# Performance work log

Measured on AMD Instinct MI355X. Metric: run time of the kernel, lower is better.

## Reference

```python
import jax, jax.numpy as jnp
import numpy as np

N = 2048
IMG = 128
FOCAL = float(IMG)


def quat_to_rot(q):
    # q = (w, x, y, z), normalized -> (N, 3, 3) rotation matrices
    q = q / jnp.linalg.norm(q, axis=-1, keepdims=True)
    w, x, y, z = q[..., 0], q[..., 1], q[..., 2], q[..., 3]
    R = jnp.stack([
        1 - 2 * (y * y + z * z), 2 * (x * y - w * z), 2 * (x * z + w * y),
        2 * (x * y + w * z), 1 - 2 * (x * x + z * z), 2 * (y * z - w * x),
        2 * (x * z - w * y), 2 * (y * z + w * x), 1 - 2 * (x * x + y * y),
    ], axis=-1).reshape(q.shape[:-1] + (3, 3))
    return R


def setup_inputs() -> dict:
    key = jax.random.key(0)
    ks = jax.random.split(key, 4)
    return {
        'means': jax.random.normal(ks[0], (N, 3), jnp.float32) * 0.5,
        'log_scales': jnp.full((N, 3), -2.0, jnp.float32) + 0.1 * jax.random.normal(ks[1], (N, 3), jnp.float32),
        'rotations': jax.random.normal(ks[2], (N, 4), jnp.float32) + jnp.array([2.0, 0.0, 0.0, 0.0], jnp.float32),
        'opacity_logit': jnp.zeros((N, 1), jnp.float32),
        'color_pre': jax.random.normal(ks[3], (N, 3), jnp.float32) * 0.5,
        'cam_pos': jnp.array([0.0, 0.0, 5.0], jnp.float32),
        'look_at': jnp.zeros((3,), jnp.float32),
    }


def reference(means, log_scales, rotations, opacity_logit, color_pre, cam_pos, look_at):
    # --- activations of learned params ---
    scales = jnp.exp(log_scales)                      # (N, 3)
    opac = jax.nn.sigmoid(opacity_logit)[:, 0]        # (N,)
    colors = jax.nn.sigmoid(color_pre)                # (N, 3)

    # --- 3D covariance: Sigma = R S S^T R^T ---
    R = quat_to_rot(rotations)                        # (N, 3, 3)
    M = R * scales[:, None, :]                        # R @ diag(s)
    cov3d = M @ jnp.swapaxes(M, -1, -2)               # (N, 3, 3)

    # --- camera basis (world -> camera) ---
    fwd = look_at - cam_pos
    fwd = fwd / jnp.linalg.norm(fwd)
    right = jnp.cross(fwd, jnp.array([0.0, 1.0, 0.0], jnp.float32))
    right = right / jnp.linalg.norm(right)
    up = jnp.cross(right, fwd)
    Wm = jnp.stack([right, up, -fwd], axis=0)         # (3, 3)

    # --- project means ---
    means_cam = (means - cam_pos[None]) @ Wm.T        # (N, 3)
    depths = -means_cam[:, 2]
    x_cam = means_cam[:, 0] / (-means_cam[:, 2] + 1e-8)
    y_cam = means_cam[:, 1] / (-means_cam[:, 2] + 1e-8)
    means_2d = jnp.stack([x_cam * FOCAL + IMG / 2, -y_cam * FOCAL + IMG / 2], axis=-1)

    # --- EWA 2D covariance ---
    cov_cam = jnp.einsum('ab,nbc,dc->nad', Wm, cov3d, Wm)      # W Sigma W^T
    z_sq = jnp.maximum(depths ** 2, 0.01)[:, None, None]
    cov_2d = cov_cam[:, :2, :2] * FOCAL ** 2 / z_sq + 0.3 * jnp.eye(2, dtype=jnp.float32)

    # --- depth sort (front to back) ---
    idx = jnp.argsort(depths)
    d_s = depths[idx]
    m2d = means_2d[idx]
    c2d = cov_2d[idx]
    col_s = colors[idx]
    op_s = opac[idx]

    # culling -> mask instead of dynamic filtering (jit-friendly, same math)
    valid = ((d_s > 0.1)
             & (m2d[:, 0] > -IMG) & (m2d[:, 0] < 2 * IMG)
             & (m2d[:, 1] > -IMG) & (m2d[:, 1] < 2 * IMG)).astype(jnp.float32)

    a = c2d[:, 0, 0]
    b = c2d[:, 0, 1]
    d = c2d[:, 1, 1]
    det = jnp.maximum(a * d - b * b, 1e-6)
    cov_inv = jnp.stack([d, -b, -b, a], axis=-1).reshape(-1, 2, 2) / det[:, None, None]

    yy, xx = jnp.meshgrid(jnp.arange(IMG, dtype=jnp.float32),
                          jnp.arange(IMG, dtype=jnp.float32), indexing='ij')
    pixels = jnp.stack([xx, yy], axis=-1)             # (H, W, 2)

    def body(carry, g):
        image, T = carry
        mu, inv, col, op, v = g
        diff = pixels - mu                            # (H, W, 2)
        mahal = jnp.einsum('hwi,ij,hwj->hw', diff, inv, diff)
        alpha = jnp.minimum(op * jnp.exp(-0.5 * mahal), 0.99) * v
        image = image + (T * alpha)[..., None] * (col[None, None] - image)
        T = T * (1.0 - alpha)
        return (image, T), None

    init = (jnp.ones((IMG, IMG, 3), jnp.float32), jnp.ones((IMG, IMG), jnp.float32))
    (image, _), _ = jax.lax.scan(body, init, (m2d, cov_inv, col_s, op_s, valid))
    return jnp.clip(image, 0.0, 1.0)
```

## Files before the change

### kernel.cpp

```cpp
#include <hip/hip_runtime.h>
#include <hip/hip_bf16.h>
#include <hip/hip_fp16.h>

#define N_G   2048
#define IMGF  128.0f
#define RECF  8


typedef __fp16 half2_v __attribute__((ext_vector_type(2)));
union H2U { half2_v h2; float f; unsigned int u; };

static __device__ __forceinline__ unsigned int f32_bf16(float f) {
    unsigned int u = __float_as_uint(f);
    return (u + 0x7FFFu + ((u >> 16) & 1u)) >> 16;
}

__global__ void gs_preprocess(const float* __restrict__ means,
                              const float* __restrict__ log_scales,
                              const float* __restrict__ rotations,
                              const float* __restrict__ opacity_logit,
                              const float* __restrict__ color_pre,
                              const float* __restrict__ cam_pos,
                              const float* __restrict__ look_at,
                              float* __restrict__ rec,
                              unsigned long long* __restrict__ keys)
{
    int i = blockIdx.x * blockDim.x + threadIdx.x;
    if (i >= N_G) return;

    float cx = cam_pos[0], cy = cam_pos[1], cz = cam_pos[2];
    float fx = look_at[0] - cx, fy = look_at[1] - cy, fz = look_at[2] - cz;
    float fn = 1.0f / sqrtf(fx*fx + fy*fy + fz*fz);
    fx *= fn; fy *= fn; fz *= fn;
    float rx = -fz, ry = 0.0f, rz = fx;
    float rn = 1.0f / sqrtf(rx*rx + ry*ry + rz*rz);
    rx *= rn; ry *= rn; rz *= rn;
    float ux = ry*fz - rz*fy, uy = rz*fx - rx*fz, uz = rx*fy - ry*fx;

    float mx = means[3*i+0] - cx, my = means[3*i+1] - cy, mz = means[3*i+2] - cz;
    float m0 =  rx*mx + ry*my + rz*mz;
    float m1 =  ux*mx + uy*my + uz*mz;
    float m2 = -(fx*mx + fy*my + fz*mz);
    float d  = -m2;
    float invz = 1.0f / (-m2 + 1e-8f);
    float m2dx =  (m0 * invz) * IMGF + IMGF * 0.5f;
    float m2dy = -(m1 * invz) * IMGF + IMGF * 0.5f;

    float s0 = expf(log_scales[3*i+0]);
    float s1 = expf(log_scales[3*i+1]);
    float s2 = expf(log_scales[3*i+2]);
    float qw = rotations[4*i+0], qx = rotations[4*i+1],
          qy = rotations[4*i+2], qz = rotations[4*i+3];
    float qn = 1.0f / sqrtf(qw*qw + qx*qx + qy*qy + qz*qz);
    qw *= qn; qx *= qn; qy *= qn; qz *= qn;
    float R00 = 1-2*(qy*qy+qz*qz), R01 = 2*(qx*qy-qw*qz), R02 = 2*(qx*qz+qw*qy);
    float R10 = 2*(qx*qy+qw*qz), R11 = 1-2*(qx*qx+qz*qz), R12 = 2*(qy*qz-qw*qx);
    float R20 = 2*(qx*qz-qw*qy), R21 = 2*(qy*qz+qw*qx), R22 = 1-2*(qx*qx+qy*qy);
    float t0 = s0*s0, t1 = s1*s1, t2 = s2*s2;
    float C00 = R00*R00*t0 + R01*R01*t1 + R02*R02*t2;
    float C01 = R00*R10*t0 + R01*R11*t1 + R02*R12*t2;
    float C02 = R00*R20*t0 + R01*R21*t1 + R02*R22*t2;
    float C11 = R10*R10*t0 + R11*R11*t1 + R12*R12*t2;
    float C12 = R10*R20*t0 + R11*R21*t1 + R12*R22*t2;
    float C22 = R20*R20*t0 + R21*R21*t1 + R22*R22*t2;

    float v0 = C00*rx + C01*ry + C02*rz;
    float v1 = C01*rx + C11*ry + C12*rz;
    float v2 = C02*rx + C12*ry + C22*rz;
    float ca = rx*v0 + ry*v1 + rz*v2;
    float cb = ux*v0 + uy*v1 + uz*v2;
    float w0 = C00*ux + C01*uy + C02*uz;
    float w1 = C01*ux + C11*uy + C12*uz;
    float w2 = C02*ux + C12*uy + C22*uz;
    float cd = ux*w0 + uy*w1 + uz*w2;

    float z2 = fmaxf(d*d, 0.01f);
    float sc = (IMGF * IMGF) / z2;
    float a  = ca*sc + 0.3f;
    float b  = cb*sc;
    float dd = cd*sc + 0.3f;
    float det  = fmaxf(a*dd - b*b, 1e-6f);
    float idet = 1.0f / det;

    bool valid = (d > 0.1f) && (m2dx > -IMGF) && (m2dx < 2.0f*IMGF)
                            && (m2dy > -IMGF) && (m2dy < 2.0f*IMGF);

    float op = 1.0f / (1.0f + expf(-opacity_logit[i]));
    const float L2E = 1.4426950408889634f;
    float A2 = -0.5f * L2E * dd * idet;
    float B2 =          L2E * b  * idet;
    float D2 = -0.5f * L2E * a  * idet;
    float L  = valid ? log2f(op) : -1e10f;

    float cr = 1.0f / (1.0f + expf(-color_pre[3*i+0]));
    float cg = 1.0f / (1.0f + expf(-color_pre[3*i+1]));
    float cl = 1.0f / (1.0f + expf(-color_pre[3*i+2]));

    unsigned int w6 = f32_bf16(cr) | (f32_bf16(cg) << 16);
    unsigned int w7 = f32_bf16(cl);

    float4* r4 = (float4*)(rec + RECF*i);
    r4[0] = make_float4(m2dx, m2dy, A2, B2);
    r4[1] = make_float4(D2, L, __uint_as_float(w6), __uint_as_float(w7));

    unsigned int ub   = __float_as_uint(d);
    unsigned int mask = ((unsigned int)((int)ub >> 31)) | 0x80000000u;
    keys[i] = ((unsigned long long)(ub ^ mask) << 32) | (unsigned int)i;
}

__global__ void __launch_bounds__(256)
gs_rank_scatter(const unsigned long long* __restrict__ keys,
                const float* __restrict__ rec,
                float* __restrict__ srec)
{
    __shared__ __align__(16) unsigned long long sk[N_G];
    int t = threadIdx.x;

    const ulonglong2* k2 = (const ulonglong2*)keys;
    ulonglong2* s2 = (ulonglong2*)sk;
    #pragma unroll
    for (int q = 0; q < 4; ++q) s2[t + q*256] = k2[t + q*256];
    __syncthreads();

    int g   = (blockIdx.x << 5) | (t >> 3);
    int seg = t & 7;
    unsigned long long ki = sk[g];
    const ulonglong2* sseg = (const ulonglong2*)(sk + (seg << 8));
    int rank = 0;
    #pragma unroll 8
    for (int j = 0; j < 128; ++j) {
        ulonglong2 a = sseg[(j + seg * 17) & 127];
        rank += (int)(a.x < ki) + (int)(a.y < ki);
    }
    rank += __shfl_xor(rank, 1);
    rank += __shfl_xor(rank, 2);
    rank += __shfl_xor(rank, 4);

    int slot = ((rank & 31) << 6) | (rank >> 5);
    srec[slot * RECF + seg] = rec[g * RECF + seg];
}

__global__ void __launch_bounds__(256, 2)
gs_raster(const float* __restrict__ srec, float* __restrict__ out)
{
    int tid  = threadIdx.x;
    int lane = tid & 63;
    int wave = (blockIdx.x << 2) | (tid >> 6);
    int p0   = wave * 2;
    float px0 = (float)(p0 & 127);
    float px1 = px0 + 1.0f;
    float py  = (float)(p0 >> 7);

    float vp[32];
    float P0 = 1.0f, P1 = 1.0f;

    #pragma unroll
    for (int i = 0; i < 32; ++i) {
        const float* r = srec + (size_t)((i << 6) | lane) * RECF;
        float4 ra = *(const float4*)r;
        float2 rb = *(const float2*)(r + 4);
        float dy   = py - ra.y;
        float b2dy = ra.w * dy;
        float t2   = fmaf(rb.x * dy, dy, rb.y);
        float dx0  = px0 - ra.x;
        float dx1  = px1 - ra.x;
        float q0 = fmaf(dx0, fmaf(ra.z, dx0, b2dy), t2);
        float q1 = fmaf(dx1, fmaf(ra.z, dx1, b2dy), t2);
        float a0 = fminf(__builtin_amdgcn_exp2f(q0), 0.99f);
        float a1 = fminf(__builtin_amdgcn_exp2f(q1), 0.99f);
        float u0 = P0 * a0;  P0 *= (1.0f - a0);
        float u1 = P1 * a1;  P1 *= (1.0f - a1);
        H2U hp; hp.h2 = __builtin_amdgcn_cvt_pkrtz(u0, u1);
        vp[i] = hp.f;
    }

    float sp0 = P0, sp1 = P1;
    #pragma unroll
    for (int d = 1; d < 64; d <<= 1) {
        float y0 = __shfl_up(sp0, d);
        float y1 = __shfl_up(sp1, d);
        if (lane >= d) { sp0 *= y0; sp1 *= y1; }
    }
    float e0 = __shfl_up(sp0, 1);
    float e1 = __shfl_up(sp1, 1);
    float Tin0 = (lane == 0) ? 1.0f : e0;
    float Tin1 = (lane == 0) ? 1.0f : e1;

    float B0 = 1.0f, B1 = 1.0f;
    #pragma unroll
    for (int i = 0; i < 32; ++i) {
        H2U h; h.f = vp[i];
        B0 *= fmaf(-Tin0, (float)h.h2.x, 1.0f);
        B1 *= fmaf(-Tin1, (float)h.h2.y, 1.0f);
    }

    float ss0 = B0, ss1 = B1;
    #pragma unroll
    for (int d = 1; d < 64; d <<= 1) {
        float y0 = __shfl_down(ss0, d);
        float y1 = __shfl_down(ss1, d);
        if (lane + d < 64) { ss0 *= y0; ss1 *= y1; }
    }
    float f0 = __shfl_down(ss0, 1);
    float f1 = __shfl_down(ss1, 1);
    float S0 = (lane == 63) ? 1.0f : f0;
    float S1 = (lane == 63) ? 1.0f : f1;

    float ar0 = 0.0f, ag0 = 0.0f, ab0 = 0.0f;
    float ar1 = 0.0f, ag1 = 0.0f, ab1 = 0.0f;
    #pragma unroll
    for (int i = 31; i >= 0; --i) {
        const float* r = srec + (size_t)((i << 6) | lane) * RECF;
        float2 cp = *(const float2*)(r + 6);
        unsigned int w6 = __float_as_uint(cp.x);
        unsigned int w7 = __float_as_uint(cp.y);
        float cr = __uint_as_float(w6 << 16);
        float cg = __uint_as_float(w6 & 0xFFFF0000u);
        float cb = __uint_as_float(w7 << 16);
        H2U h; h.f = vp[i];
        float u0  = Tin0 * (float)h.h2.x;
        float us0 = u0 * S0;
        ar0 = fmaf(us0, cr, ar0); ag0 = fmaf(us0, cg, ag0); ab0 = fmaf(us0, cb, ab0);
        S0 = fmaf(-u0, S0, S0);
        float u1  = Tin1 * (float)h.h2.y;
        float us1 = u1 * S1;
        ar1 = fmaf(us1, cr, ar1); ag1 = fmaf(us1, cg, ag1); ab1 = fmaf(us1, cb, ab1);
        S1 = fmaf(-u1, S1, S1);
    }

    #pragma unroll
    for (int d = 1; d < 64; d <<= 1) {
        ar0 += __shfl_xor(ar0, d); ag0 += __shfl_xor(ag0, d); ab0 += __shfl_xor(ab0, d);
        ar1 += __shfl_xor(ar1, d); ag1 += __shfl_xor(ab1*0.0f + ag1, d); ab1 += __shfl_xor(ab1, d);
    }

    if (lane == 0) {
        float* o0 = out + (size_t)p0 * 3;
        o0[0] = fminf(fmaxf(S0 + ar0, 0.0f), 1.0f);
        o0[1] = fminf(fmaxf(S0 + ag0, 0.0f), 1.0f);
        o0[2] = fminf(fmaxf(S0 + ab0, 0.0f), 1.0f);
        o0[3] = fminf(fmaxf(S1 + ar1, 0.0f), 1.0f);
        o0[4] = fminf(fmaxf(S1 + ag1, 0.0f), 1.0f);
        o0[5] = fminf(fmaxf(S1 + ab1, 0.0f), 1.0f);
    }
}

extern "C" void kernel_launch(void* const* d_in, const int* in_sizes, int n_in,
                              void* d_out, int out_size, void* d_ws, size_t ws_size,
                              hipStream_t stream)
{
    const float* means         = (const float*)d_in[0];
    const float* log_scales    = (const float*)d_in[1];
    const float* rotations     = (const float*)d_in[2];
    const float* opacity_logit = (const float*)d_in[3];
    const float* color_pre     = (const float*)d_in[4];
    const float* cam_pos       = (const float*)d_in[5];
    const float* look_at       = (const float*)d_in[6];
    float* out = (float*)d_out;

    char* ws = (char*)d_ws;
    float*              rec  = (float*)(ws);
    unsigned long long* keys = (unsigned long long*)(ws + 65536);
    float*              srec = (float*)(ws + 65536 + 16384);

    hipLaunchKernelGGL(gs_preprocess, dim3(N_G / 256), dim3(256), 0, stream,
                       means, log_scales, rotations, opacity_logit, color_pre,
                       cam_pos, look_at, rec, keys);
    hipLaunchKernelGGL(gs_rank_scatter, dim3(N_G / 32), dim3(256), 0, stream,
                       keys, rec, srec);
    hipLaunchKernelGGL(gs_raster, dim3(2048), dim3(256), 0, stream,
                       srec, out);
}
```

Baseline: 106.3 us.

## Process gaussians in four sequential chunks of 512 with per-chunk wave scans

The raster kernel now splits the 2048 sorted gaussians into four chunks of 512, each with its own forward transmittance scan and backward suffix scan across the wave. Results are combined across chunks through carried transmittance and a suffix-product multiplier. The sort's slot mapping changes to match the chunked layout, and the separate B-product pass is dropped. This shrinks the per-thread vp register array from 32 to 8, which lowers register pressure and the occupancy hint is relaxed accordingly, but it adds four times as many cross-lane scan rounds.

```diff
diff --git a/kernel.cpp b/kernel.cpp
--- a/kernel.cpp
+++ b/kernel.cpp
@@ -136,11 +136,11 @@
     rank += __shfl_xor(rank, 2);
     rank += __shfl_xor(rank, 4);
 
-    int slot = ((rank & 31) << 6) | (rank >> 5);
+    int slot = (rank & ~511) | ((rank & 7) << 6) | ((rank >> 3) & 63);
     srec[slot * RECF + seg] = rec[g * RECF + seg];
 }
 
-__global__ void __launch_bounds__(256, 2)
+__global__ void __launch_bounds__(256)
 gs_raster(const float* __restrict__ srec, float* __restrict__ out)
 {
     int tid  = threadIdx.x;
@@ -151,97 +151,112 @@
     float px1 = px0 + 1.0f;
     float py  = (float)(p0 >> 7);
 
-    float vp[32];
-    float P0 = 1.0f, P1 = 1.0f;
-
-    #pragma unroll
-    for (int i = 0; i < 32; ++i) {
-        const float* r = srec + (size_t)((i << 6) | lane) * RECF;
-        float4 ra = *(const float4*)r;
-        float2 rb = *(const float2*)(r + 4);
-        float dy   = py - ra.y;
-        float b2dy = ra.w * dy;
-        float t2   = fmaf(rb.x * dy, dy, rb.y);
-        float dx0  = px0 - ra.x;
-        float dx1  = px1 - ra.x;
-        float q0 = fmaf(dx0, fmaf(ra.z, dx0, b2dy), t2);
-        float q1 = fmaf(dx1, fmaf(ra.z, dx1, b2dy), t2);
-        float a0 = fminf(__builtin_amdgcn_exp2f(q0), 0.99f);
-        float a1 = fminf(__builtin_amdgcn_exp2f(q1), 0.99f);
-        float u0 = P0 * a0;  P0 *= (1.0f - a0);
-        float u1 = P1 * a1;  P1 *= (1.0f - a1);
-        H2U hp; hp.h2 = __builtin_amdgcn_cvt_pkrtz(u0, u1);
-        vp[i] = hp.f;
-    }
-
-    float sp0 = P0, sp1 = P1;
+    float G0 = 1.0f, G1 = 1.0f;
+    float Tc0 = 1.0f, Tc1 = 1.0f;
+    float Ar0 = 0.0f, Ag0 = 0.0f, Ab0 = 0.0f;
+    float Ar1 = 0.0f, Ag1 = 0.0f, Ab1 = 0.0f;
+
+    #pragma unroll 1
+    for (int r = 0; r < 4; ++r) {
+        const float* base = srec + (size_t)((r << 9) | lane) * RECF;
+
+        float vp[8];
+        float P0 = 1.0f, P1 = 1.0f;
+        #pragma unroll
+        for (int i = 0; i < 8; ++i) {
+            const float* rp = base + (size_t)(i << 6) * RECF;
+            float4 ra = *(const float4*)rp;
+            float2 rb = *(const float2*)(rp + 4);
+            float dy   = py - ra.y;
+            float b2dy = ra.w * dy;
+            float t2   = fmaf(rb.x * dy, dy, rb.y);
+            float dx0  = px0 - ra.x;
+            float dx1  = px1 - ra.x;
+            float q0 = fmaf(dx0, fmaf(ra.z, dx0, b2dy), t2);
+            float q1 = fmaf(dx1, fmaf(ra.z, dx1, b2dy), t2);
+            float a0 = fminf(__builtin_amdgcn_exp2f(q0), 0.99f);
+            float a1 = fminf(__builtin_amdgcn_exp2f(q1), 0.99f);
+            float u0 = P0 * a0;  P0 *= (1.0f - a0);
+            float u1 = P1 * a1;  P1 *= (1.0f - a1);
+            H2U hp; hp.h2 = __builtin_amdgcn_cvt_pkrtz(u0, u1);
+            vp[i] = hp.f;
+        }
+
+        float sp0 = P0, sp1 = P1;
+        #pragma unroll
+        for (int d = 1; d < 64; d <<= 1) {
+            float y0 = __shfl_up(sp0, d);
+            float y1 = __shfl_up(sp1, d);
+            if (lane >= d) { sp0 *= y0; sp1 *= y1; }
+        }
+        float e0 = __shfl_up(sp0, 1);
+        float e1 = __shfl_up(sp1, 1);
+        float Tin0 = Tc0 * ((lane == 0) ? 1.0f : e0);
+        float Tin1 = Tc1 * ((lane == 0) ? 1.0f : e1);
+        float tot0 = __shfl(sp0, 63);
+        float tot1 = __shfl(sp1, 63);
+
+        float Sl0 = 1.0f, Sl1 = 1.0f;
+        float cr0 = 0.0f, cg0 = 0.0f, cb0 = 0.0f;
+        float cr1 = 0.0f, cg1 = 0.0f, cb1 = 0.0f;
+        #pragma unroll
+        for (int i = 7; i >= 0; --i) {
+            const float* rp = base + (size_t)(i << 6) * RECF;
+            float2 cp = *(const float2*)(rp + 6);
+            unsigned int w6 = __float_as_uint(cp.x);
+            unsigned int w7 = __float_as_uint(cp.y);
+            float ccr = __uint_as_float(w6 << 16);
+            float ccg = __uint_as_float(w6 & 0xFFFF0000u);
+            float ccb = __uint_as_float(w7 << 16);
+            H2U h; h.f = vp[i];
+            float u0  = Tin0 * (float)h.h2.x;
+            float us0 = u0 * Sl0;
+            cr0 = fmaf(us0, ccr, cr0); cg0 = fmaf(us0, ccg, cg0); cb0 = fmaf(us0, ccb, cb0);
+            Sl0 = fmaf(-u0, Sl0, Sl0);
+            float u1  = Tin1 * (float)h.h2.y;
+            float us1 = u1 * Sl1;
+            cr1 = fmaf(us1, ccr, cr1); cg1 = fmaf(us1, ccg, cg1); cb1 = fmaf(us1, ccb, cb1);
+            Sl1 = fmaf(-u1, Sl1, Sl1);
+        }
+
+        float ss0 = Sl0, ss1 = Sl1;
+        #pragma unroll
+        for (int d = 1; d < 64; d <<= 1) {
+            float y0 = __shfl_down(ss0, d);
+            float y1 = __shfl_down(ss1, d);
+            if (lane + d < 64) { ss0 *= y0; ss1 *= y1; }
+        }
+        float f0 = __shfl_down(ss0, 1);
+        float f1 = __shfl_down(ss1, 1);
+        float So0 = (lane == 63) ? 1.0f : f0;
+        float So1 = (lane == 63) ? 1.0f : f1;
+        float M0 = __shfl(ss0, 0);
+        float M1 = __shfl(ss1, 0);
+
+        Ar0 = fmaf(Ar0, M0, cr0 * So0);
+        Ag0 = fmaf(Ag0, M0, cg0 * So0);
+        Ab0 = fmaf(Ab0, M0, cb0 * So0);
+        Ar1 = fmaf(Ar1, M1, cr1 * So1);
+        Ag1 = fmaf(Ag1, M1, cg1 * So1);
+        Ab1 = fmaf(Ab1, M1, cb1 * So1);
+        G0 *= M0;  G1 *= M1;
+        Tc0 *= tot0;  Tc1 *= tot1;
+    }
+
     #pragma unroll
     for (int d = 1; d < 64; d <<= 1) {
-        float y0 = __shfl_up(sp0, d);
-        float y1 = __shfl_up(sp1, d);
-        if (lane >= d) { sp0 *= y0; sp1 *= y1; }
-    }
-    float e0 = __shfl_up(sp0, 1);
-    float e1 = __shfl_up(sp1, 1);
-    float Tin0 = (lane == 0) ? 1.0f : e0;
-    float Tin1 = (lane == 0) ? 1.0f : e1;
-
-    float B0 = 1.0f, B1 = 1.0f;
-    #pragma unroll
-    for (int i = 0; i < 32; ++i) {
-        H2U h; h.f = vp[i];
-        B0 *= fmaf(-Tin0, (float)h.h2.x, 1.0f);
-        B1 *= fmaf(-Tin1, (float)h.h2.y, 1.0f);
-    }
-
-    float ss0 = B0, ss1 = B1;
-    #pragma unroll
-    for (int d = 1; d < 64; d <<= 1) {
-        float y0 = __shfl_down(ss0, d);
-        float y1 = __shfl_down(ss1, d);
-        if (lane + d < 64) { ss0 *= y0; ss1 *= y1; }
-    }
-    float f0 = __shfl_down(ss0, 1);
-    float f1 = __shfl_down(ss1, 1);
-    float S0 = (lane == 63) ? 1.0f : f0;
-    float S1 = (lane == 63) ? 1.0f : f1;
-
-    float ar0 = 0.0f, ag0 = 0.0f, ab0 = 0.0f;
-    float ar1 = 0.0f, ag1 = 0.0f, ab1 = 0.0f;
-    #pragma unroll
-    for (int i = 31; i >= 0; --i) {
-        const float* r = srec + (size_t)((i << 6) | lane) * RECF;
-        float2 cp = *(const float2*)(r + 6);
-        unsigned int w6 = __float_as_uint(cp.x);
-        unsigned int w7 = __float_as_uint(cp.y);
-        float cr = __uint_as_float(w6 << 16);
-        float cg = __uint_as_float(w6 & 0xFFFF0000u);
-        float cb = __uint_as_float(w7 << 16);
-        H2U h; h.f = vp[i];
-        float u0  = Tin0 * (float)h.h2.x;
-        float us0 = u0 * S0;
-        ar0 = fmaf(us0, cr, ar0); ag0 = fmaf(us0, cg, ag0); ab0 = fmaf(us0, cb, ab0);
-        S0 = fmaf(-u0, S0, S0);
-        float u1  = Tin1 * (float)h.h2.y;
-        float us1 = u1 * S1;
-        ar1 = fmaf(us1, cr, ar1); ag1 = fmaf(us1, cg, ag1); ab1 = fmaf(us1, cb, ab1);
-        S1 = fmaf(-u1, S1, S1);
-    }
-
-    #pragma unroll
-    for (int d = 1; d < 64; d <<= 1) {
-        ar0 += __shfl_xor(ar0, d); ag0 += __shfl_xor(ag0, d); ab0 += __shfl_xor(ab0, d);
-        ar1 += __shfl_xor(ar1, d); ag1 += __shfl_xor(ab1*0.0f + ag1, d); ab1 += __shfl_xor(ab1, d);
+        Ar0 += __shfl_xor(Ar0, d); Ag0 += __shfl_xor(Ag0, d); Ab0 += __shfl_xor(Ab0, d);
+        Ar1 += __shfl_xor(Ar1, d); Ag1 += __shfl_xor(Ag1, d); Ab1 += __shfl_xor(Ab1, d);
     }
 
     if (lane == 0) {
         float* o0 = out + (size_t)p0 * 3;
-        o0[0] = fminf(fmaxf(S0 + ar0, 0.0f), 1.0f);
-        o0[1] = fminf(fmaxf(S0 + ag0, 0.0f), 1.0f);
-        o0[2] = fminf(fmaxf(S0 + ab0, 0.0f), 1.0f);
-        o0[3] = fminf(fmaxf(S1 + ar1, 0.0f), 1.0f);
-        o0[4] = fminf(fmaxf(S1 + ag1, 0.0f), 1.0f);
-        o0[5] = fminf(fmaxf(S1 + ab1, 0.0f), 1.0f);
+        o0[0] = fminf(fmaxf(G0 + Ar0, 0.0f), 1.0f);
+        o0[1] = fminf(fmaxf(G0 + Ag0, 0.0f), 1.0f);
+        o0[2] = fminf(fmaxf(G0 + Ab0, 0.0f), 1.0f);
+        o0[3] = fminf(fmaxf(G1 + Ar1, 0.0f), 1.0f);
+        o0[4] = fminf(fmaxf(G1 + Ag1, 0.0f), 1.0f);
+        o0[5] = fminf(fmaxf(G1 + Ab1, 0.0f), 1.0f);
     }
 }
 
```

Measured after the change: 99.01 us. 6.9% less time.
